# Optimization experiments

Hardware: AMD Instinct MI355X
Metric: run time of the kernel (lower is better)

The kernel has to match this reference:

```python
import jax, jax.numpy as jnp
import numpy as np

B, S, DIN, DH = 8, 8192, 256, 256


def setup_inputs() -> dict:
    key = jax.random.key(0)
    k0, k1, k2, k3, k4 = jax.random.split(key, 5)
    stdv = 1.0 / np.sqrt(DIN)
    x = jax.random.normal(k0, (B, S, DIN), jnp.float32)
    W0 = jax.random.uniform(k1, (2 * DH, DIN), jnp.float32, -stdv, stdv)
    b0 = jax.random.uniform(k2, (2 * DH,), jnp.float32, -stdv, stdv)
    stdv2 = 1.0 / np.sqrt(DH)
    W1 = jax.random.uniform(k3, (2 * DH, DH), jnp.float32, -stdv2, stdv2)
    b1 = jax.random.uniform(k4, (2 * DH,), jnp.float32, -stdv2, stdv2)
    return {"x": x, "W0": W0, "b0": b0, "W1": W1, "b1": b1}


def _log_g(x):
    # log of g(x) = x + 0.5 for x >= 0 else sigmoid(x)
    return jnp.where(x >= 0, jnp.log(jax.nn.relu(x) + 0.5), -jax.nn.softplus(-x))


def _mingru_layer(x, W, b):
    # x: (B,S,Din); W: (2*DH, Din); b: (2*DH,)
    gh = jnp.einsum('bsd,ed->bse', x, W) + b          # (B,S,2*DH)
    gate, hidden = jnp.split(gh, 2, axis=-1)          # each (B,S,DH)
    log_coeffs = -jax.nn.softplus(gate)               # log(1 - z)
    log_vals = -jax.nn.softplus(-gate) + _log_g(hidden)  # log z + log h_tilde
    Bb, Ss, Dd = log_coeffs.shape
    # initial hidden h0 = g(0) = 0.5  ->  log(h0) = log(0.5)
    log_h0 = jnp.full((Bb, 1, Dd), jnp.log(0.5), log_coeffs.dtype)
    log_values = jnp.concatenate([log_h0, log_vals], axis=1)          # (B,S+1,DH)
    a_star = jnp.concatenate(
        [jnp.zeros((Bb, 1, Dd), log_coeffs.dtype), jnp.cumsum(log_coeffs, axis=1)],
        axis=1)                                                       # (B,S+1,DH)
    log_h = a_star + jax.lax.cumlogsumexp(log_values - a_star, axis=1)
    return jnp.exp(log_h)[:, 1:]                                      # (B,S,DH)


def reference(x, W0, b0, W1, b1):
    out0 = _mingru_layer(x, W0, b0)
    out1 = _mingru_layer(out0, W1, b1)
    h = jnp.stack([out0[:, -1:], out1[:, -1:]])  # (num_layers,B,1,DH)
    return out1, h
```

## Files before the change

kernel.cpp:

```cpp
#include <hip/hip_runtime.h>
#include <hip/hip_bf16.h>

#define Bb 8
#define Ss 8192
#define Dd 256
#define Mm (Bb * Ss)
#define Nn 512
#define NCHUNK 128
#define CLEN (Ss / NCHUNK)

typedef __hip_bfloat16 bf16;
typedef __attribute__((ext_vector_type(8))) short short8;
typedef __attribute__((ext_vector_type(4))) float f32x4;

__device__ __forceinline__ void load_lds16(const void* g, void* l) {
  __builtin_amdgcn_global_load_lds(
      (const __attribute__((address_space(1))) void*)g,
      (__attribute__((address_space(3))) void*)l, 16, 0, 0);
}

template <int N>
__device__ __forceinline__ void wait_vmcnt() {
  if constexpr (N == 0)
    asm volatile("s_waitcnt vmcnt(0)" ::: "memory");
  else if constexpr (N == 4)
    asm volatile("s_waitcnt vmcnt(4)" ::: "memory");
  else if constexpr (N == 6)
    asm volatile("s_waitcnt vmcnt(6)" ::: "memory");
  else
    static_assert(N == 0 || N == 4 || N == 6, "unsupported vmcnt");
}

__global__ __launch_bounds__(256) void cvt_f32_bf16(const float* __restrict__ in,
                                                    bf16* __restrict__ out,
                                                    long n4) {
  long i = (long)blockIdx.x * blockDim.x + threadIdx.x;
  if (i >= n4) return;
  const float4 v = ((const float4*)in)[i];
  union { ushort4 u; bf16 h[4]; } o;
  o.h[0] = __float2bfloat16(v.x);
  o.h[1] = __float2bfloat16(v.y);
  o.h[2] = __float2bfloat16(v.z);
  o.h[3] = __float2bfloat16(v.w);
  ((ushort4*)out)[i] = o.u;
}

__device__ __forceinline__ void av_from_gh(float gate, float hid, float& a,
                                           float& v) {
  gate = fminf(fmaxf(gate, -20.f), 20.f);
  float eg = __expf(gate);
  a = 1.f / (1.f + eg);
  float z = eg * a;
  float gfun;
  if (hid >= 0.f) {
    gfun = hid + 0.5f;
  } else {
    float eh = __expf(fmaxf(hid, -20.f));
    gfun = eh / (1.f + eh);
  }
  v = z * gfun;
}

__device__ __forceinline__ unsigned pack_av(float a, float v) {
  union { bf16 h[2]; unsigned u; } o;
  o.h[0] = __float2bfloat16(a);
  o.h[1] = __float2bfloat16(v);
  return o.u;
}

template <bool F32A>
__global__ __launch_bounds__(256) void gemm_av_fused(
    const void* __restrict__ Xv, const bf16* __restrict__ W,
    const float* __restrict__ bias, unsigned* __restrict__ AV,
    float* __restrict__ Asum, float* __restrict__ Vsum) {
  constexpr int ABY = F32A ? 16384 : 8192;
  constexpr int NLD = F32A ? 6 : 4;
  __shared__ __align__(16) char sm[2 * ABY + 16384];
  char* Abuf0 = sm;
  char* Abuf1 = sm + ABY;
  bf16* Bbuf0 = (bf16*)(sm + 2 * ABY);
  bf16* Bbuf1 = (bf16*)(sm + 2 * ABY + 8192);
  unsigned* Ts = (unsigned*)sm;

  const int tid = threadIdx.x;
  const int w = tid >> 6;
  const int l = tid & 63;
  const int fl = l & 15;
  const int q = l >> 4;

  const int id = blockIdx.x;
  const int lin = ((id & 7) << 8) | (id >> 3);
  const int cb = lin & 3;
  const int bt = lin >> 2;
  const long rowBase = (long)bt * 128;
  const int wrow = (w >> 1) * 64;
  const int wc = (w & 1) * 32;

  const float* Xf = (const float*)Xv;
  const bf16* Xb = (const bf16*)Xv;

  auto stageA = [&](char* dst, int k0) {
    if constexpr (F32A) {
#pragma unroll
      for (int c = 0; c < 4; c++) {
        const int L = c * 256 + tid;
        const int row = L >> 3;
        const int kc = (L & 7) ^ (row & 7);
        load_lds16(Xf + (rowBase + row) * 256 + k0 + kc * 4,
                   dst + (c * 256 + w * 64) * 16);
      }
    } else {
#pragma unroll
      for (int c = 0; c < 2; c++) {
        const int L = c * 256 + tid;
        const int row = L >> 2;
        const int kc = (L & 3) ^ ((row >> 1) & 3);
        load_lds16(Xb + (rowBase + row) * 256 + k0 + kc * 8,
                   dst + (c * 256 + w * 64) * 16);
      }
    }
  };
  auto stageB = [&](bf16* dst, int k0) {
#pragma unroll
    for (int c = 0; c < 2; c++) {
      const int L = c * 256 + tid;
      const int row = L >> 2;
      const int kc = (L & 3) ^ ((row >> 1) & 3);
      const int grow = (row < 64) ? (cb * 64 + row) : (192 + cb * 64 + row);
      load_lds16(W + (long)grow * 256 + k0 + kc * 8,
                 (char*)dst + (c * 256 + w * 64) * 16);
    }
  };

  auto fragA = [&](const char* buf, int mt) -> short8 {
    const int row = wrow + 16 * mt + fl;
    if constexpr (F32A) {
      const float* p = (const float*)buf + row * 32;
      const int k0c = (2 * q) ^ (row & 7);
      const int k1c = (2 * q + 1) ^ (row & 7);
      const float4 u0 = *(const float4*)(p + k0c * 4);
      const float4 u1 = *(const float4*)(p + k1c * 4);
      const float vals[8] = {u0.x, u0.y, u0.z, u0.w, u1.x, u1.y, u1.z, u1.w};
      short8 r;
#pragma unroll
      for (int i = 0; i < 8; i++) {
        union { bf16 h; short s; } t;
        t.h = __float2bfloat16(vals[i]);
        r[i] = t.s;
      }
      return r;
    } else {
      const int kc = q ^ ((row >> 1) & 3);
      return *(const short8*)((const bf16*)buf + row * 32 + kc * 8);
    }
  };
  auto fragB = [&](const bf16* buf, int nt) -> short8 {
    const int row =
        (nt < 2) ? (wc + 16 * nt + fl) : (64 + wc + 16 * (nt - 2) + fl);
    const int kc = q ^ ((row >> 1) & 3);
    return *(const short8*)(buf + row * 32 + kc * 8);
  };

  f32x4 acc[4][4];
#pragma unroll
  for (int i = 0; i < 4; i++)
#pragma unroll
    for (int j = 0; j < 4; j++) acc[i][j] = (f32x4)0.0f;

  stageA(Abuf0, 0);
  stageB(Bbuf0, 0);
  stageA(Abuf1, 32);
  stageB(Bbuf1, 32);
#pragma unroll
  for (int ks = 0; ks < 8; ks++) {
    char* Ac = (ks & 1) ? Abuf1 : Abuf0;
    bf16* Bc = (ks & 1) ? Bbuf1 : Bbuf0;
    if (ks < 7)
      wait_vmcnt<NLD>();
    else
      wait_vmcnt<0>();
    __builtin_amdgcn_s_barrier();
    __builtin_amdgcn_sched_barrier(0);
    short8 af[4], bf_[4];
#pragma unroll
    for (int mt = 0; mt < 4; mt++) af[mt] = fragA(Ac, mt);
#pragma unroll
    for (int nt = 0; nt < 4; nt++) bf_[nt] = fragB(Bc, nt);
#pragma unroll
    for (int mt = 0; mt < 4; mt++)
#pragma unroll
      for (int nt = 0; nt < 4; nt++)
        acc[mt][nt] = __builtin_amdgcn_mfma_f32_16x16x32_bf16(
            af[mt], bf_[nt], acc[mt][nt], 0, 0, 0);
    asm volatile("s_waitcnt lgkmcnt(0)" ::: "memory");
    __builtin_amdgcn_s_barrier();
    if (ks < 6) {
      stageA(Ac, (ks + 2) * 32);
      stageB(Bc, (ks + 2) * 32);
    }
  }

  float bg[2], bh[2];
#pragma unroll
  for (int p = 0; p < 2; p++) {
    const int d = cb * 64 + wc + 16 * p + fl;
    bg[p] = bias[d];
    bh[p] = bias[256 + d];
  }
  unsigned pk[4][2][4];
#pragma unroll
  for (int mt = 0; mt < 4; mt++) {
#pragma unroll
    for (int p = 0; p < 2; p++) {
      const int d = cb * 64 + wc + 16 * p + fl;
      const long r0 = rowBase + wrow + 16 * mt + q * 4;
#pragma unroll
      for (int r = 0; r < 4; r++) {
        float a, v;
        av_from_gh(acc[mt][p][r] + bg[p], acc[mt][p + 2][r] + bh[p], a, v);
        pk[mt][p][r] = pack_av(a, v);
        AV[(r0 + r) * 256 + d] = pk[mt][p][r];
      }
    }
  }

#pragma unroll
  for (int h = 0; h < 2; h++) {
    if ((w >> 1) == h) {
#pragma unroll
      for (int mt = 0; mt < 4; mt++)
#pragma unroll
        for (int p = 0; p < 2; p++)
#pragma unroll
          for (int r = 0; r < 4; r++)
            Ts[(16 * mt + 4 * q + r) * 65 + wc + 16 * p + fl] = pk[mt][p][r];
    }
    __syncthreads();
    if (tid < 64) {
      float A = 1.f, H = 0.f;
#pragma unroll 8
      for (int t = 0; t < 64; t++) {
        const unsigned p = Ts[t * 65 + tid];
        const float a = __uint_as_float((p & 0xffffu) << 16);
        const float v = __uint_as_float(p & 0xffff0000u);
        A *= a;
        H = a * H + v;
      }
      const long cg = (long)(bt >> 6) * NCHUNK + ((bt & 63) << 1) + h;
      Asum[cg * 256 + cb * 64 + tid] = A;
      Vsum[cg * 256 + cb * 64 + tid] = H;
    }
    __syncthreads();
  }
}

__global__ __launch_bounds__(256) void scan_combine(
    const float* __restrict__ Asum, const float* __restrict__ Vsum,
    float* __restrict__ Hin) {
  const int d = threadIdx.x;
  const int b = blockIdx.x;
  float h = 0.5f;
#pragma unroll 8
  for (int c = 0; c < NCHUNK; c++) {
    const long i = ((long)b * NCHUNK + c) * 256 + d;
    Hin[i] = h;
    h = Asum[i] * h + Vsum[i];
  }
}

template <bool WRITE_BF16>
__global__ __launch_bounds__(256) void scan_final(
    const unsigned* __restrict__ AV, const float* __restrict__ Hin,
    bf16* __restrict__ OutB, float* __restrict__ OutF,
    float* __restrict__ Hlast) {
  const int d = threadIdx.x;
  const int c = blockIdx.x % NCHUNK;
  const int b = blockIdx.x / NCHUNK;
  float h = Hin[(long)blockIdx.x * 256 + d];
  long base = ((long)b * Ss + (long)c * CLEN) * 256 + d;
#pragma unroll 8
  for (int t = 0; t < CLEN; t++) {
    const unsigned p = AV[base];
    const float a = __uint_as_float((p & 0xffffu) << 16);
    const float v = __uint_as_float(p & 0xffff0000u);
    h = a * h + v;
    if (WRITE_BF16)
      OutB[base] = __float2bfloat16(h);
    else
      OutF[base] = h;
    base += 256;
  }
  if (c == NCHUNK - 1) Hlast[b * 256 + d] = h;
}

extern "C" void kernel_launch(void* const* d_in, const int* in_sizes, int n_in,
                              void* d_out, int out_size, void* d_ws,
                              size_t ws_size, hipStream_t stream) {
  const float* x = (const float*)d_in[0];
  const float* W0f = (const float*)d_in[1];
  const float* b0 = (const float*)d_in[2];
  const float* W1f = (const float*)d_in[3];
  const float* b1 = (const float*)d_in[4];

  float* outF = (float*)d_out;
  float* hlast = outF + (long)Mm * 256;
  bf16* Xb = (bf16*)d_out;

  char* ws = (char*)d_ws;
  unsigned* AV = (unsigned*)ws;
  bf16* W0b = (bf16*)(ws + (long)Mm * 256 * 4);
  bf16* W1b = W0b + (long)Nn * Dd;
  float* Asum = (float*)(W1b + (long)Nn * Dd);
  float* Vsum = Asum + (long)Bb * NCHUNK * 256;
  float* Hin = Vsum + (long)Bb * NCHUNK * 256;

  const dim3 gemmGrid(2048);
  const dim3 blk(256);
  const dim3 scanGrid(Bb * NCHUNK);

  {
    const long n4w = (long)Nn * Dd / 4;
    cvt_f32_bf16<<<dim3((n4w + 255) / 256), blk, 0, stream>>>(W0f, W0b, n4w);
    cvt_f32_bf16<<<dim3((n4w + 255) / 256), blk, 0, stream>>>(W1f, W1b, n4w);
  }

  gemm_av_fused<true><<<gemmGrid, blk, 0, stream>>>(x, W0b, b0, AV, Asum,
                                                    Vsum);
  scan_combine<<<dim3(Bb), blk, 0, stream>>>(Asum, Vsum, Hin);
  scan_final<true><<<scanGrid, blk, 0, stream>>>(AV, Hin, Xb, nullptr, hlast);

  gemm_av_fused<false><<<gemmGrid, blk, 0, stream>>>(Xb, W1b, b1, AV, Asum,
                                                     Vsum);
  scan_combine<<<dim3(Bb), blk, 0, stream>>>(Asum, Vsum, Hin);
  scan_final<false><<<scanGrid, blk, 0, stream>>>(AV, Hin, nullptr, outF,
                                                  hlast + Bb * 256);
}
```

Before: 267.0 us.

## Drop scan_combine kernel, coalesce AV stores via LDS, fuse weight conversions

Removes the serial scan_combine launch. Each scan_final block instead recomputes its chunk's starting state by folding the packed (A,H) chunk summaries of all earlier chunks. The GEMM epilogue now stages AV through the padded LDS tile and writes it as coalesced uint4 rows in a column-blocked layout, and scan_final reads that layout. The two weight conversions are merged into one launch, staging address math is precomputed, and occupancy hints are added. The trade-off is redundant prefix work in later chunks, up to 127 sequential steps per block.

```diff
diff --git a/kernel.cpp b/kernel.cpp
--- a/kernel.cpp
+++ b/kernel.cpp
@@ -8,6 +8,7 @@
 #define Nn 512
 #define NCHUNK 128
 #define CLEN (Ss / NCHUNK)
+#define TSP 68
 
 typedef __hip_bfloat16 bf16;
 typedef __attribute__((ext_vector_type(8))) short short8;
@@ -31,11 +32,18 @@
     static_assert(N == 0 || N == 4 || N == 6, "unsupported vmcnt");
 }
 
-__global__ __launch_bounds__(256) void cvt_f32_bf16(const float* __restrict__ in,
-                                                    bf16* __restrict__ out,
-                                                    long n4) {
+__global__ __launch_bounds__(256) void cvt_weights(
+    const float* __restrict__ inA, const float* __restrict__ inB,
+    bf16* __restrict__ outA, bf16* __restrict__ outB, long n4each) {
   long i = (long)blockIdx.x * blockDim.x + threadIdx.x;
-  if (i >= n4) return;
+  const float* in = inA;
+  bf16* out = outA;
+  if (i >= n4each) {
+    in = inB;
+    out = outB;
+    i -= n4each;
+  }
+  if (i >= n4each) return;
   const float4 v = ((const float4*)in)[i];
   union { ushort4 u; bf16 h[4]; } o;
   o.h[0] = __float2bfloat16(v.x);
@@ -51,13 +59,9 @@
   float eg = __expf(gate);
   a = 1.f / (1.f + eg);
   float z = eg * a;
-  float gfun;
-  if (hid >= 0.f) {
-    gfun = hid + 0.5f;
-  } else {
-    float eh = __expf(fmaxf(hid, -20.f));
-    gfun = eh / (1.f + eh);
-  }
+  float eh = __expf(fminf(fmaxf(hid, -20.f), 0.f));
+  float sig = eh / (1.f + eh);
+  float gfun = (hid >= 0.f) ? (hid + 0.5f) : sig;
   v = z * gfun;
 }
 
@@ -69,17 +73,15 @@
 }
 
 template <bool F32A>
-__global__ __launch_bounds__(256) void gemm_av_fused(
+__global__ __launch_bounds__(256, F32A ? 3 : 5) void gemm_av_fused(
     const void* __restrict__ Xv, const bf16* __restrict__ W,
     const float* __restrict__ bias, unsigned* __restrict__ AV,
-    float* __restrict__ Asum, float* __restrict__ Vsum) {
+    float2* __restrict__ AVs) {
   constexpr int ABY = F32A ? 16384 : 8192;
   constexpr int NLD = F32A ? 6 : 4;
   __shared__ __align__(16) char sm[2 * ABY + 16384];
-  char* Abuf0 = sm;
-  char* Abuf1 = sm + ABY;
-  bf16* Bbuf0 = (bf16*)(sm + 2 * ABY);
-  bf16* Bbuf1 = (bf16*)(sm + 2 * ABY + 8192);
+  char* Ab[2] = {sm, sm + ABY};
+  bf16* Bbf[2] = {(bf16*)(sm + 2 * ABY), (bf16*)(sm + 2 * ABY + 8192)};
   unsigned* Ts = (unsigned*)sm;
 
   const int tid = threadIdx.x;
@@ -99,37 +101,50 @@
   const float* Xf = (const float*)Xv;
   const bf16* Xb = (const bf16*)Xv;
 
-  auto stageA = [&](char* dst, int k0) {
-    if constexpr (F32A) {
-#pragma unroll
-      for (int c = 0; c < 4; c++) {
-        const int L = c * 256 + tid;
-        const int row = L >> 3;
-        const int kc = (L & 7) ^ (row & 7);
-        load_lds16(Xf + (rowBase + row) * 256 + k0 + kc * 4,
-                   dst + (c * 256 + w * 64) * 16);
-      }
-    } else {
-#pragma unroll
-      for (int c = 0; c < 2; c++) {
-        const int L = c * 256 + tid;
-        const int row = L >> 2;
-        const int kc = (L & 3) ^ ((row >> 1) & 3);
-        load_lds16(Xb + (rowBase + row) * 256 + k0 + kc * 8,
-                   dst + (c * 256 + w * 64) * 16);
-      }
-    }
-  };
-  auto stageB = [&](bf16* dst, int k0) {
+  const float* aSrcF[4];
+  const bf16* aSrcB[2];
+  const bf16* bSrc[2];
+  int aDstF[4], sDst[2];
+  if constexpr (F32A) {
+#pragma unroll
+    for (int c = 0; c < 4; c++) {
+      const int L = c * 256 + tid;
+      const int row = L >> 3;
+      const int kc = (L & 7) ^ (row & 7);
+      aSrcF[c] = Xf + (rowBase + row) * 256 + kc * 4;
+      aDstF[c] = (c * 256 + w * 64) * 16;
+    }
+  } else {
 #pragma unroll
     for (int c = 0; c < 2; c++) {
       const int L = c * 256 + tid;
       const int row = L >> 2;
       const int kc = (L & 3) ^ ((row >> 1) & 3);
-      const int grow = (row < 64) ? (cb * 64 + row) : (192 + cb * 64 + row);
-      load_lds16(W + (long)grow * 256 + k0 + kc * 8,
-                 (char*)dst + (c * 256 + w * 64) * 16);
-    }
+      aSrcB[c] = Xb + (rowBase + row) * 256 + kc * 8;
+    }
+  }
+#pragma unroll
+  for (int c = 0; c < 2; c++) {
+    const int L = c * 256 + tid;
+    const int row = L >> 2;
+    const int kc = (L & 3) ^ ((row >> 1) & 3);
+    const int grow = (row < 64) ? (cb * 64 + row) : (192 + cb * 64 + row);
+    bSrc[c] = W + (long)grow * 256 + kc * 8;
+    sDst[c] = (c * 256 + w * 64) * 16;
+  }
+  auto stage = [&](int bi, int ks) {
+    if constexpr (F32A) {
+#pragma unroll
+      for (int c = 0; c < 4; c++)
+        load_lds16(aSrcF[c] + ks * 32, Ab[bi] + aDstF[c]);
+    } else {
+#pragma unroll
+      for (int c = 0; c < 2; c++)
+        load_lds16(aSrcB[c] + ks * 32, Ab[bi] + sDst[c]);
+    }
+#pragma unroll
+    for (int c = 0; c < 2; c++)
+      load_lds16(bSrc[c] + ks * 32, (char*)Bbf[bi] + sDst[c]);
   };
 
   auto fragA = [&](const char* buf, int mt) -> short8 {
@@ -167,14 +182,11 @@
 #pragma unroll
     for (int j = 0; j < 4; j++) acc[i][j] = (f32x4)0.0f;
 
-  stageA(Abuf0, 0);
-  stageB(Bbuf0, 0);
-  stageA(Abuf1, 32);
-  stageB(Bbuf1, 32);
+  stage(0, 0);
+  stage(1, 1);
 #pragma unroll
   for (int ks = 0; ks < 8; ks++) {
-    char* Ac = (ks & 1) ? Abuf1 : Abuf0;
-    bf16* Bc = (ks & 1) ? Bbuf1 : Bbuf0;
+    const int bi = ks & 1;
     if (ks < 7)
       wait_vmcnt<NLD>();
     else
@@ -183,9 +195,9 @@
     __builtin_amdgcn_sched_barrier(0);
     short8 af[4], bf_[4];
 #pragma unroll
-    for (int mt = 0; mt < 4; mt++) af[mt] = fragA(Ac, mt);
-#pragma unroll
-    for (int nt = 0; nt < 4; nt++) bf_[nt] = fragB(Bc, nt);
+    for (int mt = 0; mt < 4; mt++) af[mt] = fragA(Ab[bi], mt);
+#pragma unroll
+    for (int nt = 0; nt < 4; nt++) bf_[nt] = fragB(Bbf[bi], nt);
 #pragma unroll
     for (int mt = 0; mt < 4; mt++)
 #pragma unroll
@@ -194,10 +206,8 @@
             af[mt], bf_[nt], acc[mt][nt], 0, 0, 0);
     asm volatile("s_waitcnt lgkmcnt(0)" ::: "memory");
     __builtin_amdgcn_s_barrier();
-    if (ks < 6) {
-      stageA(Ac, (ks + 2) * 32);
-      stageB(Bc, (ks + 2) * 32);
-    }
+    __builtin_amdgcn_sched_barrier(0);
+    if (ks < 6) stage(bi, ks + 2);
   }
 
   float bg[2], bh[2];
@@ -209,20 +219,15 @@
   }
   unsigned pk[4][2][4];
 #pragma unroll
-  for (int mt = 0; mt < 4; mt++) {
-#pragma unroll
-    for (int p = 0; p < 2; p++) {
-      const int d = cb * 64 + wc + 16 * p + fl;
-      const long r0 = rowBase + wrow + 16 * mt + q * 4;
+  for (int mt = 0; mt < 4; mt++)
+#pragma unroll
+    for (int p = 0; p < 2; p++)
 #pragma unroll
       for (int r = 0; r < 4; r++) {
         float a, v;
         av_from_gh(acc[mt][p][r] + bg[p], acc[mt][p + 2][r] + bh[p], a, v);
         pk[mt][p][r] = pack_av(a, v);
-        AV[(r0 + r) * 256 + d] = pk[mt][p][r];
       }
-    }
-  }
 
 #pragma unroll
   for (int h = 0; h < 2; h++) {
@@ -233,62 +238,67 @@
         for (int p = 0; p < 2; p++)
 #pragma unroll
           for (int r = 0; r < 4; r++)
-            Ts[(16 * mt + 4 * q + r) * 65 + wc + 16 * p + fl] = pk[mt][p][r];
+            Ts[(16 * mt + 4 * q + r) * TSP + wc + 16 * p + fl] = pk[mt][p][r];
     }
     __syncthreads();
+    {
+      unsigned* dst = AV + ((long)cb * Mm + rowBase + h * 64) * 64;
+#pragma unroll
+      for (int j = 0; j < 4; j++) {
+        const int idx = j * 256 + tid;
+        const int t = idx >> 4;
+        const int d4 = idx & 15;
+        const uint4 val = *(const uint4*)(Ts + t * TSP + d4 * 4);
+        *(uint4*)(dst + 4 * idx) = val;
+      }
+    }
     if (tid < 64) {
       float A = 1.f, H = 0.f;
 #pragma unroll 8
       for (int t = 0; t < 64; t++) {
-        const unsigned p = Ts[t * 65 + tid];
+        const unsigned p = Ts[t * TSP + tid];
         const float a = __uint_as_float((p & 0xffffu) << 16);
         const float v = __uint_as_float(p & 0xffff0000u);
         A *= a;
         H = a * H + v;
       }
       const long cg = (long)(bt >> 6) * NCHUNK + ((bt & 63) << 1) + h;
-      Asum[cg * 256 + cb * 64 + tid] = A;
-      Vsum[cg * 256 + cb * 64 + tid] = H;
+      AVs[cg * 256 + cb * 64 + tid] = make_float2(A, H);
     }
     __syncthreads();
-  }
-}
-
-__global__ __launch_bounds__(256) void scan_combine(
-    const float* __restrict__ Asum, const float* __restrict__ Vsum,
-    float* __restrict__ Hin) {
-  const int d = threadIdx.x;
-  const int b = blockIdx.x;
-  float h = 0.5f;
-#pragma unroll 8
-  for (int c = 0; c < NCHUNK; c++) {
-    const long i = ((long)b * NCHUNK + c) * 256 + d;
-    Hin[i] = h;
-    h = Asum[i] * h + Vsum[i];
   }
 }
 
 template <bool WRITE_BF16>
 __global__ __launch_bounds__(256) void scan_final(
-    const unsigned* __restrict__ AV, const float* __restrict__ Hin,
+    const unsigned* __restrict__ AV, const float2* __restrict__ AVs,
     bf16* __restrict__ OutB, float* __restrict__ OutF,
     float* __restrict__ Hlast) {
   const int d = threadIdx.x;
   const int c = blockIdx.x % NCHUNK;
   const int b = blockIdx.x / NCHUNK;
-  float h = Hin[(long)blockIdx.x * 256 + d];
-  long base = ((long)b * Ss + (long)c * CLEN) * 256 + d;
+
+  float h = 0.5f;
+#pragma unroll 4
+  for (int j = 0; j < c; j++) {
+    const float2 av = AVs[((long)b * NCHUNK + j) * 256 + d];
+    h = av.x * h + av.y;
+  }
+
+  const long row0 = (long)b * Ss + (long)c * CLEN;
+  const unsigned* src = AV + (long)(d >> 6) * Mm * 64 + (d & 63);
+  long obase = row0 * 256 + d;
 #pragma unroll 8
   for (int t = 0; t < CLEN; t++) {
-    const unsigned p = AV[base];
+    const unsigned p = src[(row0 + t) * 64];
     const float a = __uint_as_float((p & 0xffffu) << 16);
     const float v = __uint_as_float(p & 0xffff0000u);
     h = a * h + v;
     if (WRITE_BF16)
-      OutB[base] = __float2bfloat16(h);
+      OutB[obase] = __float2bfloat16(h);
     else
-      OutF[base] = h;
-    base += 256;
+      OutF[obase] = h;
+    obase += 256;
   }
   if (c == NCHUNK - 1) Hlast[b * 256 + d] = h;
 }
@@ -304,34 +314,26 @@
 
   float* outF = (float*)d_out;
   float* hlast = outF + (long)Mm * 256;
-  bf16* Xb = (bf16*)d_out;
+  bf16* X1b = (bf16*)d_out;
 
   char* ws = (char*)d_ws;
   unsigned* AV = (unsigned*)ws;
   bf16* W0b = (bf16*)(ws + (long)Mm * 256 * 4);
   bf16* W1b = W0b + (long)Nn * Dd;
-  float* Asum = (float*)(W1b + (long)Nn * Dd);
-  float* Vsum = Asum + (long)Bb * NCHUNK * 256;
-  float* Hin = Vsum + (long)Bb * NCHUNK * 256;
+  float2* AVs = (float2*)(W1b + (long)Nn * Dd);
 
   const dim3 gemmGrid(2048);
   const dim3 blk(256);
-  const dim3 scanGrid(Bb * NCHUNK);
-
-  {
-    const long n4w = (long)Nn * Dd / 4;
-    cvt_f32_bf16<<<dim3((n4w + 255) / 256), blk, 0, stream>>>(W0f, W0b, n4w);
-    cvt_f32_bf16<<<dim3((n4w + 255) / 256), blk, 0, stream>>>(W1f, W1b, n4w);
-  }
-
-  gemm_av_fused<true><<<gemmGrid, blk, 0, stream>>>(x, W0b, b0, AV, Asum,
-                                                    Vsum);
-  scan_combine<<<dim3(Bb), blk, 0, stream>>>(Asum, Vsum, Hin);
-  scan_final<true><<<scanGrid, blk, 0, stream>>>(AV, Hin, Xb, nullptr, hlast);
-
-  gemm_av_fused<false><<<gemmGrid, blk, 0, stream>>>(Xb, W1b, b1, AV, Asum,
-                                                     Vsum);
-  scan_combine<<<dim3(Bb), blk, 0, stream>>>(Asum, Vsum, Hin);
-  scan_final<false><<<scanGrid, blk, 0, stream>>>(AV, Hin, nullptr, outF,
-                                                  hlast + Bb * 256);
-}
+
+  const long n4w = (long)Nn * Dd / 4;
+  cvt_weights<<<dim3((2 * n4w + 255) / 256), blk, 0, stream>>>(W0f, W1f, W0b,
+                                                               W1b, n4w);
+
+  gemm_av_fused<true><<<gemmGrid, blk, 0, stream>>>(x, W0b, b0, AV, AVs);
+  scan_final<true><<<dim3(Bb * NCHUNK), blk, 0, stream>>>(AV, AVs, X1b,
+                                                          nullptr, hlast);
+
+  gemm_av_fused<false><<<gemmGrid, blk, 0, stream>>>(X1b, W1b, b1, AV, AVs);
+  scan_final<false><<<dim3(Bb * NCHUNK), blk, 0, stream>>>(
+      AV, AVs, nullptr, outF, hlast + Bb * 256);
+}
```

After: 277.5 us. 3.9% more time.
